# Kernel tuning notes

Hardware: AMD Instinct MI355X
Metric: run time of the kernel (lower is better)

## Reference

```python
import jax, jax.numpy as jnp
import numpy as np

# fatigue class -> emotion target distribution; row 3 is the uniform fallback
_TABLE = np.array([
    [0.05, 0.02, 0.03, 0.4, 0.05, 0.4, 0.05],
    [0.05, 0.05, 0.05, 0.05, 0.3, 0.05, 0.45],
    [0.1, 0.15, 0.2, 0.02, 0.35, 0.03, 0.15],
    [1.0 / 7.0] * 7,
], dtype=np.float32)

B = 4_000_000

def setup_inputs() -> dict:
    key = jax.random.key(0)
    k1, k2, k3 = jax.random.split(key, 3)
    fatigue_logits = jax.random.normal(k1, (B, 3), dtype=jnp.float32)
    emotion_logits = jax.random.normal(k2, (B, 7), dtype=jnp.float32)
    fatigue_targets = jax.random.randint(k3, (B,), 0, 4, dtype=jnp.int64)
    return {"fatigue_logits": fatigue_logits,
            "emotion_logits": emotion_logits,
            "fatigue_targets": fatigue_targets}

def reference(fatigue_logits, emotion_logits, fatigue_targets):
    eps = 1e-8
    table = jnp.asarray(_TABLE)
    # targets outside {0,1,2} map to the uniform row (index 3)
    idx = jnp.where((fatigue_targets >= 0) & (fatigue_targets <= 2), fatigue_targets, 3)
    target = table[idx]                      # [B, 7] gather from tiny LUT
    target = target + eps
    target = target / jnp.sum(target, axis=-1, keepdims=True)
    probs = jax.nn.softmax(emotion_logits, axis=-1)
    log_input = jnp.log(probs + eps)
    # F.kl_div(log_input, target, reduction='batchmean')
    kl = jnp.sum(target * (jnp.log(target) - log_input)) / target.shape[0]
    return kl
```

## Files before the change

kernel.cpp:

```cpp
#include <hip/hip_runtime.h>
#include <cmath>

struct KLC {
    float w0[7], w1[7], w2[7], w3[7];
    float cst0, cst1, cst2, cst3;
};

typedef __attribute__((ext_vector_type(4))) float f4;
typedef __attribute__((ext_vector_type(4))) int   i4;

__device__ __forceinline__ void row_part(
    float x0, float x1, float x2, float x3, float x4, float x5, float x6,
    int t, const KLC& kc, float& lin, float& Z)
{
    int c = ((unsigned)t <= 2u) ? t : 3;

    Z = __expf(x0) + __expf(x1) + __expf(x2) + __expf(x3)
      + __expf(x4) + __expf(x5) + __expf(x6);

    float d0 = fmaf(kc.w0[6], x6, fmaf(kc.w0[5], x5, fmaf(kc.w0[4], x4,
               fmaf(kc.w0[3], x3, fmaf(kc.w0[2], x2, fmaf(kc.w0[1], x1, kc.w0[0] * x0))))));
    float d1 = fmaf(kc.w1[6], x6, fmaf(kc.w1[5], x5, fmaf(kc.w1[4], x4,
               fmaf(kc.w1[3], x3, fmaf(kc.w1[2], x2, fmaf(kc.w1[1], x1, kc.w1[0] * x0))))));
    float d2 = fmaf(kc.w2[6], x6, fmaf(kc.w2[5], x5, fmaf(kc.w2[4], x4,
               fmaf(kc.w2[3], x3, fmaf(kc.w2[2], x2, fmaf(kc.w2[1], x1, kc.w2[0] * x0))))));
    float d3 = fmaf(kc.w3[6], x6, fmaf(kc.w3[5], x5, fmaf(kc.w3[4], x4,
               fmaf(kc.w3[3], x3, fmaf(kc.w3[2], x2, fmaf(kc.w3[1], x1, kc.w3[0] * x0))))));

    float dw = (c == 0) ? d0 : (c == 1) ? d1 : (c == 2) ? d2 : d3;
    float cs = (c == 0) ? kc.cst0 : (c == 1) ? kc.cst1 : (c == 2) ? kc.cst2 : kc.cst3;
    lin = cs - dw;
}

__device__ __forceinline__ float quad_kl(
    f4 c0, f4 c1, f4 c2, f4 c3, f4 c4, f4 c5, f4 c6, i4 tq, const KLC& kc)
{
    float l0, l1, l2, l3, Z0, Z1, Z2, Z3;
    row_part(c0.x, c0.y, c0.z, c0.w, c1.x, c1.y, c1.z, tq.x, kc, l0, Z0);
    row_part(c1.w, c2.x, c2.y, c2.z, c2.w, c3.x, c3.y, tq.y, kc, l1, Z1);
    row_part(c3.z, c3.w, c4.x, c4.y, c4.z, c4.w, c5.x, tq.z, kc, l2, Z2);
    row_part(c5.y, c5.z, c5.w, c6.x, c6.y, c6.z, c6.w, tq.w, kc, l3, Z3);
    return l0 + l1 + l2 + l3 + __logf((Z0 * Z1) * (Z2 * Z3));
}

__global__ __launch_bounds__(256) void kl_main(
    const float* __restrict__ logits,
    const int*   __restrict__ tgt,
    int nchunks,
    double* __restrict__ partial,
    KLC kc)
{
    __shared__ f4 lds[4 * 448 + 4];
    const int lane = threadIdx.x & 63;
    const int wave = threadIdx.x >> 6;
    f4* const myl = &lds[wave * 448];

    const f4* __restrict__ lg = (const f4*)logits;
    const i4* __restrict__ tg = (const i4*)tgt;

    const int gwave  = blockIdx.x * 4 + wave;
    const int nwaves = gridDim.x * 4;

    float local = 0.0f;
    for (int ch = gwave; ch < nchunks; ch += nwaves) {
        asm volatile("s_waitcnt lgkmcnt(0)" ::: "memory");

        const long long base4 = (long long)ch * 448;
        #pragma unroll
        for (int k = 0; k < 7; ++k) {
            __builtin_amdgcn_global_load_lds(
                (const __attribute__((address_space(1))) void*)(lg + base4 + k * 64 + lane),
                (__attribute__((address_space(3))) void*)(myl + k * 64),
                16, 0, 0);
        }
        i4 tq = tg[(long long)ch * 64 + lane];

        asm volatile("s_waitcnt vmcnt(0)" ::: "memory");

        f4 c0 = myl[lane * 7 + 0];
        f4 c1 = myl[lane * 7 + 1];
        f4 c2 = myl[lane * 7 + 2];
        f4 c3 = myl[lane * 7 + 3];
        f4 c4 = myl[lane * 7 + 4];
        f4 c5 = myl[lane * 7 + 5];
        f4 c6 = myl[lane * 7 + 6];

        local += quad_kl(c0, c1, c2, c3, c4, c5, c6, tq, kc);
    }

    #pragma unroll
    for (int off = 32; off > 0; off >>= 1)
        local += __shfl_down(local, off, 64);

    __shared__ float smem[4];
    if (lane == 0) smem[wave] = local;
    __syncthreads();
    if (threadIdx.x == 0)
        partial[blockIdx.x] = (double)(smem[0] + smem[1] + smem[2] + smem[3]);
}

__global__ __launch_bounds__(256) void kl_reduce(
    const float* __restrict__ logits,
    const int*   __restrict__ tgt,
    long long tail_start, int tail,
    const double* __restrict__ partial, int nb,
    float* __restrict__ out, int B, KLC kc)
{
    double s = 0.0;
    for (int i = threadIdx.x; i < nb; i += 256) s += partial[i];

    float tl = 0.0f;
    for (int r = threadIdx.x; r < tail; r += 256) {
        const float* x = logits + (tail_start + r) * 7;
        float lin, Z;
        row_part(x[0], x[1], x[2], x[3], x[4], x[5], x[6],
                 tgt[tail_start + r], kc, lin, Z);
        tl += lin + __logf(Z);
    }
    s += (double)tl;

    #pragma unroll
    for (int off = 32; off > 0; off >>= 1)
        s += __shfl_down(s, off, 64);

    __shared__ double smem[4];
    int lane = threadIdx.x & 63;
    int wid  = threadIdx.x >> 6;
    if (lane == 0) smem[wid] = s;
    __syncthreads();
    if (threadIdx.x == 0)
        out[0] = (float)((smem[0] + smem[1] + smem[2] + smem[3]) / (double)B);
}

extern "C" void kernel_launch(void* const* d_in, const int* in_sizes, int n_in,
                              void* d_out, int out_size, void* d_ws, size_t ws_size,
                              hipStream_t stream) {
    const float* emotion = (const float*)d_in[1];
    const int*   targets = (const int*)d_in[2];
    float*  out     = (float*)d_out;
    double* partial = (double*)d_ws;

    const int B = in_sizes[2];
    const int nchunks = B / 256;
    const int tail = B - nchunks * 256;
    const long long tail_start = (long long)nchunks * 256;

    int nb = 1280;
    if ((size_t)nb * sizeof(double) > ws_size)
        nb = (int)(ws_size / sizeof(double));

    static const double T[4][7] = {
        {0.05, 0.02, 0.03, 0.4, 0.05, 0.4, 0.05},
        {0.05, 0.05, 0.05, 0.05, 0.3, 0.05, 0.45},
        {0.1, 0.15, 0.2, 0.02, 0.35, 0.03, 0.15},
        {1.0/7.0, 1.0/7.0, 1.0/7.0, 1.0/7.0, 1.0/7.0, 1.0/7.0, 1.0/7.0},
    };
    const double eps = 1e-8;
    KLC kc;
    float* wrows[4] = { kc.w0, kc.w1, kc.w2, kc.w3 };
    float* csts[4]  = { &kc.cst0, &kc.cst1, &kc.cst2, &kc.cst3 };
    for (int c = 0; c < 4; ++c) {
        double s = 0.0;
        for (int j = 0; j < 7; ++j) s += T[c][j] + eps;
        double cst = 0.0;
        for (int j = 0; j < 7; ++j) {
            double w = (T[c][j] + eps) / s;
            wrows[c][j] = (float)w;
            cst += w * std::log(w);
        }
        *csts[c] = (float)cst;
    }

    kl_main<<<nb, 256, 0, stream>>>(emotion, targets, nchunks, partial, kc);
    kl_reduce<<<1, 256, 0, stream>>>(emotion, targets, tail_start, tail,
                                     partial, nb, out, B, kc);
}
```

Measured before the change: 196.1 us.

## Double-buffer LDS staging of logits chunks and shrink the grid

The main loop now prefetches the next chunk of logits and targets into a second per-wave LDS buffer while computing on the current one. It waits with a partial vmcnt so only the older loads must finish, which overlaps memory latency with the softmax/KL arithmetic. The change doubles LDS per block and cuts the grid from 1280 to 512 blocks, with launch bounds hinting two blocks per CU. That lowers the number of resident waves, so there is less parallelism across waves in exchange for deeper prefetch within each wave.

```diff
diff --git a/kernel.cpp b/kernel.cpp
--- a/kernel.cpp
+++ b/kernel.cpp
@@ -43,17 +43,30 @@
     return l0 + l1 + l2 + l3 + __logf((Z0 * Z1) * (Z2 * Z3));
 }
 
-__global__ __launch_bounds__(256) void kl_main(
+__device__ __forceinline__ void stage7(const f4* __restrict__ lg, long long base4,
+                                       f4* dst, int lane)
+{
+    #pragma unroll
+    for (int k = 0; k < 7; ++k) {
+        __builtin_amdgcn_global_load_lds(
+            (const __attribute__((address_space(1))) void*)(lg + base4 + k * 64 + lane),
+            (__attribute__((address_space(3))) void*)(dst + k * 64),
+            16, 0, 0);
+    }
+}
+
+__global__ __launch_bounds__(256, 2) void kl_main(
     const float* __restrict__ logits,
     const int*   __restrict__ tgt,
     int nchunks,
     double* __restrict__ partial,
     KLC kc)
 {
-    __shared__ f4 lds[4 * 448 + 4];
+    __shared__ f4 lds[8 * 448];
     const int lane = threadIdx.x & 63;
     const int wave = threadIdx.x >> 6;
-    f4* const myl = &lds[wave * 448];
+    f4* const bufA = &lds[wave * 448];
+    f4* const bufB = &lds[(wave + 4) * 448];
 
     const f4* __restrict__ lg = (const f4*)logits;
     const i4* __restrict__ tg = (const i4*)tgt;
@@ -62,30 +75,40 @@
     const int nwaves = gridDim.x * 4;
 
     float local = 0.0f;
-    for (int ch = gwave; ch < nchunks; ch += nwaves) {
-        asm volatile("s_waitcnt lgkmcnt(0)" ::: "memory");
-
-        const long long base4 = (long long)ch * 448;
-        #pragma unroll
-        for (int k = 0; k < 7; ++k) {
-            __builtin_amdgcn_global_load_lds(
-                (const __attribute__((address_space(1))) void*)(lg + base4 + k * 64 + lane),
-                (__attribute__((address_space(3))) void*)(myl + k * 64),
-                16, 0, 0);
+    int ch = gwave;
+    if (ch < nchunks) {
+        stage7(lg, (long long)ch * 448, bufA, lane);
+        i4 tq_cur = tg[(long long)ch * 64 + lane];
+
+        f4* cur = bufA;
+        f4* nxt = bufB;
+        while (true) {
+            const int  nc  = ch + nwaves;
+            const bool has = nc < nchunks;
+            i4 tq_next;
+            if (has) {
+                stage7(lg, (long long)nc * 448, nxt, lane);
+                tq_next = tg[(long long)nc * 64 + lane];
+                asm volatile("s_waitcnt vmcnt(8)" ::: "memory");
+            } else {
+                asm volatile("s_waitcnt vmcnt(0)" ::: "memory");
+            }
+
+            f4 c0 = cur[lane * 7 + 0];
+            f4 c1 = cur[lane * 7 + 1];
+            f4 c2 = cur[lane * 7 + 2];
+            f4 c3 = cur[lane * 7 + 3];
+            f4 c4 = cur[lane * 7 + 4];
+            f4 c5 = cur[lane * 7 + 5];
+            f4 c6 = cur[lane * 7 + 6];
+
+            local += quad_kl(c0, c1, c2, c3, c4, c5, c6, tq_cur, kc);
+
+            if (!has) break;
+            ch = nc;
+            f4* t = cur; cur = nxt; nxt = t;
+            tq_cur = tq_next;
         }
-        i4 tq = tg[(long long)ch * 64 + lane];
-
-        asm volatile("s_waitcnt vmcnt(0)" ::: "memory");
-
-        f4 c0 = myl[lane * 7 + 0];
-        f4 c1 = myl[lane * 7 + 1];
-        f4 c2 = myl[lane * 7 + 2];
-        f4 c3 = myl[lane * 7 + 3];
-        f4 c4 = myl[lane * 7 + 4];
-        f4 c5 = myl[lane * 7 + 5];
-        f4 c6 = myl[lane * 7 + 6];
-
-        local += quad_kl(c0, c1, c2, c3, c4, c5, c6, tq, kc);
     }
 
     #pragma unroll
@@ -145,7 +168,7 @@
     const int tail = B - nchunks * 256;
     const long long tail_start = (long long)nchunks * 256;
 
-    int nb = 1280;
+    int nb = 512;
     if ((size_t)nb * sizeof(double) > ws_size)
         nb = (int)(ws_size / sizeof(double));
 
```

Result: no change. 197.3 us (+0.6%).
